# Kernel optimization log

Hardware: AMD Instinct MI355X
Metric: run time of the kernel (lower is better)

Reference implementation:

```python
import jax, jax.numpy as jnp
import numpy as np
from jax import lax

B = 64      # batch (n_image == n_caption)
R = 36      # image regions
W = 32      # words per caption (uniform cap_lens)
D = 1024    # embedding dim
LAMBDA_SOFTMAX = 9.0
LAMBDA_LSE = 6.0
ALPHA = 0.1
MARGIN = 0.2
OT_ITER = 20
BETA = 0.5
EPS = 1e-8


def setup_inputs() -> dict:
    key = jax.random.key(0)
    k1, k2, k3 = jax.random.split(key, 3)
    im = jax.random.normal(k1, (B, R, D), jnp.float32)
    s = jax.random.normal(k2, (B, W, D), jnp.float32)
    x = jax.random.normal(k3, (B, W, D), jnp.float32)
    s_l = jnp.full((B,), W, dtype=jnp.int32)
    return {"im": im, "s": s, "s_l": s_l, "x": x}


def _l2norm(a, axis):
    # matches torch l2norm: x / (sqrt(sum(x^2)) + eps)
    return a / (jnp.sqrt(jnp.sum(a * a, axis=axis, keepdims=True)) + EPS)


def _scores_t2i(im, s, x):
    # ---- func_attention (t2i): query = caption words, context = image regions ----
    # raw attn: (c, i, r, w) = context @ query^T for every caption/image pair
    attn = jnp.einsum('ird,cwd->cirw', im, s)
    attn = jax.nn.leaky_relu(attn, negative_slope=0.1)   # clipped_l2norm
    attn = _l2norm(attn, axis=3)                          # l2norm over query (word) axis
    attn = jnp.swapaxes(attn, 2, 3)                       # (c, i, w, r)
    attn = jax.nn.softmax(attn * LAMBDA_SOFTMAX, axis=3)  # softmax over regions
    wctx = jnp.einsum('ciwr,ird->ciwd', attn, im)         # weighted context (c,i,w,d)

    # cosine similarity between caption words and weighted context, over d
    num = jnp.einsum('cwd,ciwd->ciw', s, wctx)
    w1 = jnp.linalg.norm(s, axis=2)[:, None, :]           # (c,1,w)
    w2 = jnp.linalg.norm(wctx, axis=3)                    # (c,i,w)
    row_sim = num / jnp.maximum(w1 * w2, EPS)             # (c,i,w)

    # LogSumExp aggregation over words
    sim = jax.nn.logsumexp(row_sim * LAMBDA_LSE, axis=2) / LAMBDA_LSE  # (c,i)

    # ---- OT cost matrix: cosine distance between x words and image regions ----
    xn = x / (jnp.linalg.norm(x, axis=2, keepdims=True) + 1e-12)
    imn = im / (jnp.linalg.norm(im, axis=2, keepdims=True) + 1e-12)
    C = 1.0 - jnp.einsum('cwd,ird->ciwr', xn, imn)        # (c,i,W,R)

    # ---- IPOT (uniform marginals, beta=0.5, one inner step) ----
    A = jnp.exp(-C / BETA)
    T0 = jnp.ones_like(C)
    sigma0 = jnp.full(C.shape[:2] + (R,), 1.0 / R, dtype=C.dtype)

    def body(carry, _):
        T, sigma = carry
        Q = A * T                                          # (c,i,W,R)
        delta = 1.0 / (W * jnp.einsum('ciwr,cir->ciw', Q, sigma))
        sigma = 1.0 / (R * jnp.einsum('ciwr,ciw->cir', Q, delta))
        T = delta[..., :, None] * Q * sigma[..., None, :]
        return (T, sigma), None

    (T, _), _ = lax.scan(body, (T0, sigma0), None, length=OT_ITER)
    ot_dist = jnp.sum(C * T, axis=(-2, -1))               # trace(C^T T) -> (c,i)
    ot_sim = -ot_dist

    # torch code concatenates per-caption columns: scores[img, cap]
    return sim.T, ot_sim.T                                 # (n_img, n_cap)


def reference(im, s, s_l, x):
    # s_l is uniform (== W); the per-caption slicing in the torch loop is a no-op.
    scores, scores_ot = _scores_t2i(im, s, x)
    n = scores.shape[0]

    diag = jnp.diagonal(scores)
    diag_ot = jnp.diagonal(scores_ot)

    cost_s = jnp.maximum(MARGIN + scores - diag[:, None], 0.0)
    cost_im = jnp.maximum(MARGIN + scores - diag[None, :], 0.0)
    cost_s_ot = jnp.maximum(MARGIN + scores_ot - diag_ot[:, None], 0.0)
    cost_im_ot = jnp.maximum(MARGIN + scores_ot - diag_ot[None, :], 0.0)

    off = 1.0 - jnp.eye(n, dtype=scores.dtype)
    cost_s = cost_s * off
    cost_im = cost_im * off
    cost_s_ot = cost_s_ot * off
    cost_im_ot = cost_im_ot * off

    cost_s = cost_s + ALPHA * cost_s_ot
    cost_im = cost_im + ALPHA * cost_im_ot

    # max_violation = True
    cost_s = jnp.max(cost_s, axis=1)
    cost_im = jnp.max(cost_im, axis=0)
    cost_s_ot = jnp.max(cost_s_ot, axis=1)
    cost_im_ot = jnp.max(cost_im_ot, axis=0)

    return (jnp.sum(cost_s) + jnp.sum(cost_im),
            jnp.sum(cost_s_ot) + jnp.sum(cost_im_ot))
```

## Files before the change

kernel.cpp:

```cpp
#include <hip/hip_runtime.h>
#include <cstdint>
#include <cstddef>


typedef __attribute__((ext_vector_type(8))) short short8;
typedef __attribute__((ext_vector_type(4))) float f32x4;
typedef __attribute__((ext_vector_type(2))) float f2;

__device__ __forceinline__ unsigned short f2bf(float f) {
  unsigned u = __float_as_uint(f);
  u += 0x7FFFu + ((u >> 16) & 1u);
  return (unsigned short)(u >> 16);
}
__device__ __forceinline__ float rcpf(float x) { return __builtin_amdgcn_rcpf(x); }

__global__ __launch_bounds__(256) void k_prep(const float* __restrict__ s,
                                              const float* __restrict__ x,
                                              const float* __restrict__ im,
                                              unsigned short* __restrict__ Ab,
                                              unsigned short* __restrict__ Bb,
                                              float* __restrict__ w1,
                                              float* __restrict__ xn_r,
                                              float* __restrict__ imn_r) {
  int row = blockIdx.x, tid = threadIdx.x;
  const float* src; unsigned short* dst; float* np; int recip;
  if (row < 2048)      { src = s  + (size_t)row * 1024;          dst = Ab + (size_t)row * 1024;          np = w1    + row;          recip = 0; }
  else if (row < 4096) { src = x  + (size_t)(row - 2048) * 1024; dst = Ab + (size_t)row * 1024;          np = xn_r  + (row - 2048); recip = 1; }
  else                 { src = im + (size_t)(row - 4096) * 1024; dst = Bb + (size_t)(row - 4096) * 1024; np = imn_r + (row - 4096); recip = 1; }
  float4 f = ((const float4*)src)[tid];
  ushort4 h;
  h.x = f2bf(f.x); h.y = f2bf(f.y); h.z = f2bf(f.z); h.w = f2bf(f.w);
  ((ushort4*)dst)[tid] = h;
  float p = f.x*f.x + f.y*f.y + f.z*f.z + f.w*f.w;
  #pragma unroll
  for (int o = 32; o > 0; o >>= 1) p += __shfl_down(p, o, 64);
  __shared__ float red[4];
  if ((tid & 63) == 0) red[tid >> 6] = p;
  __syncthreads();
  if (tid == 0) {
    float n = sqrtf(red[0] + red[1] + red[2] + red[3]);
    *np = recip ? 1.f / (n + 1e-12f) : n;
  }
}

__global__ __launch_bounds__(256) void k_gram(const float* __restrict__ im,
                                              float* __restrict__ G) {
  int b = blockIdx.x, r = blockIdx.y;
  int wid = threadIdx.x >> 6, l = threadIdx.x & 63;
  const float* rowr = im + ((size_t)b*36 + r) * 1024;
  float4 my[4];
  #pragma unroll
  for (int j = 0; j < 4; ++j) my[j] = ((const float4*)rowr)[j*64 + l];
  float* Gr = G + ((size_t)b*36 + r) * 36;
  for (int rp = wid; rp < 36; rp += 4) {
    const float* rowp = im + ((size_t)b*36 + rp) * 1024;
    float p = 0.f;
    #pragma unroll
    for (int j = 0; j < 4; ++j) {
      float4 u = ((const float4*)rowp)[j*64 + l];
      p += my[j].x*u.x + my[j].y*u.y + my[j].z*u.z + my[j].w*u.w;
    }
    #pragma unroll
    for (int o = 32; o > 0; o >>= 1) p += __shfl_down(p, o, 64);
    if (l == 0) Gr[rp] = p;
  }
}

__global__ __launch_bounds__(256) void k_gemm_mfma(const unsigned short* __restrict__ A,
                                                   const unsigned short* __restrict__ B,
                                                   unsigned short* __restrict__ dot) {
  __shared__ unsigned short lA[128 * 32];
  __shared__ unsigned short lB[96 * 32];
  int tid = threadIdx.x;
  int bn = blockIdx.x * 96, bm = blockIdx.y * 128;
  int wid = tid >> 6, l = tid & 63;
  int wr = (wid >> 1) * 64, wc = (wid & 1) * 48;
  int lr = l & 15, lq = l >> 4;

  f32x4 acc[4][3] = {};

  int row_a = tid >> 2;
  int kq = (tid & 3) * 8;
  const unsigned short* gA = A + (size_t)(bm + row_a) * 1024 + kq;
  const unsigned short* gB = B + (size_t)(bn + row_a) * 1024 + kq;
  unsigned loff = (unsigned)tid * 16u;

  for (int kt = 0; kt < 1024; kt += 32) {
    __builtin_amdgcn_global_load_lds(
        (const __attribute__((address_space(1))) void*)(gA + kt),
        (__attribute__((address_space(3))) void*)((char*)lA + loff), 16, 0, 0);
    __builtin_amdgcn_global_load_lds(
        (const __attribute__((address_space(1))) void*)(gA + 64*1024 + kt),
        (__attribute__((address_space(3))) void*)((char*)lA + 4096 + loff), 16, 0, 0);
    __builtin_amdgcn_global_load_lds(
        (const __attribute__((address_space(1))) void*)(gB + kt),
        (__attribute__((address_space(3))) void*)((char*)lB + loff), 16, 0, 0);
    if (tid < 128)
      __builtin_amdgcn_global_load_lds(
          (const __attribute__((address_space(1))) void*)(gB + 64*1024 + kt),
          (__attribute__((address_space(3))) void*)((char*)lB + 4096 + loff), 16, 0, 0);
    __syncthreads();

    short8 af[4], bfr[3];
    #pragma unroll
    for (int mi = 0; mi < 4; ++mi)
      af[mi] = *(const short8*)&lA[(wr + mi*16 + lr) * 32 + lq * 8];
    #pragma unroll
    for (int ni = 0; ni < 3; ++ni)
      bfr[ni] = *(const short8*)&lB[(wc + ni*16 + lr) * 32 + lq * 8];
    #pragma unroll
    for (int mi = 0; mi < 4; ++mi)
      #pragma unroll
      for (int ni = 0; ni < 3; ++ni)
        acc[mi][ni] = __builtin_amdgcn_mfma_f32_16x16x32_bf16(af[mi], bfr[ni], acc[mi][ni], 0, 0, 0);
    __syncthreads();
  }

  #pragma unroll
  for (int mi = 0; mi < 4; ++mi)
    #pragma unroll
    for (int ni = 0; ni < 3; ++ni) {
      int gcol = bn + wc + ni*16 + lr;
      #pragma unroll
      for (int q = 0; q < 4; ++q) {
        int grow = bm + wr + mi*16 + lq*4 + q;
        dot[(size_t)grow * 2304 + gcol] = f2bf(acc[mi][ni][q]);
      }
    }
}

template<int C>
__device__ __forceinline__ float dpp_add(float v) {
  return v + __int_as_float(__builtin_amdgcn_mov_dpp(__float_as_int(v), C, 0xF, 0xF, true));
}
template<int C>
__device__ __forceinline__ float dpp_max(float v) {
  return fmaxf(v, __int_as_float(__builtin_amdgcn_mov_dpp(__float_as_int(v), C, 0xF, 0xF, true)));
}
__device__ __forceinline__ float bsum32(float v) {
  v = dpp_add<0xB1>(v);
  v = dpp_add<0x4E>(v);
  v = dpp_add<0x141>(v);
  v = dpp_add<0x128>(v);
  v += __shfl_xor(v, 16, 64);
  return v;
}
__device__ __forceinline__ float bmax32(float v) {
  v = dpp_max<0xB1>(v);
  v = dpp_max<0x4E>(v);
  v = dpp_max<0x141>(v);
  v = dpp_max<0x128>(v);
  v = fmaxf(v, __shfl_xor(v, 16, 64));
  return v;
}

__global__ __launch_bounds__(256, 4) void k_pair(const unsigned short* __restrict__ dotb,
                                                 const float* __restrict__ Gm,
                                                 const float* __restrict__ w1m,
                                                 const float* __restrict__ xnrm,
                                                 const float* __restrict__ imnrm,
                                                 float* __restrict__ S,
                                                 float* __restrict__ Sot) {
  int wid  = threadIdx.x >> 6;
  int pair = blockIdx.x * 4 + wid;
  int c = pair >> 6, i = pair & 63;
  int l = threadIdx.x & 63;
  int h = l >> 5, w = l & 31;
  int r0 = h * 18;

  const unsigned* drow = (const unsigned*)(dotb + (size_t)(c*32 + w) * 2304 + i*36 + r0);
  const unsigned* xrow = (const unsigned*)((const unsigned short*)drow + (size_t)2048 * 2304);
  float w1  = w1m[c*32 + w];
  float xnr = xnrm[c*32 + w];

  f2 d2[9], Cm2[9];
  #pragma unroll
  for (int k = 0; k < 9; ++k) {
    unsigned u = drow[k];
    d2[k][0] = __uint_as_float(u << 16);
    d2[k][1] = __uint_as_float(u & 0xFFFF0000u);
  }
  const f2* ir = (const f2*)(imnrm + i*36 + r0);
  #pragma unroll
  for (int k = 0; k < 9; ++k) {
    unsigned u = xrow[k];
    f2 xv;
    xv[0] = __uint_as_float(u << 16);
    xv[1] = __uint_as_float(u & 0xFFFF0000u);
    xv *= xnr;
    Cm2[k] = 1.f - xv * ir[k];
  }

  f2 f[9];
  #pragma unroll
  for (int k = 0; k < 9; ++k) {
    f2 t = d2[k] * 0.1f;
    f[k][0] = fmaxf(d2[k][0], t[0]);
    f[k][1] = fmaxf(d2[k][1], t[1]);
  }
  f2 p2[9];
  #pragma unroll
  for (int k = 0; k < 9; ++k) {
    f2 sq = f[k] * f[k];
    float t0 = bsum32(sq[0]);
    float t1 = bsum32(sq[1]);
    f2 rs;
    rs[0] = __builtin_amdgcn_rsqf(fmaxf(t0 * 0.012345679f, 1e-30f));
    rs[1] = __builtin_amdgcn_rsqf(fmaxf(t1 * 0.012345679f, 1e-30f));
    p2[k] = f[k] * rs;
  }
  float mx = fmaxf(fmaxf(p2[0][0], p2[0][1]), fmaxf(p2[1][0], p2[1][1]));
  #pragma unroll
  for (int k = 2; k < 9; ++k) mx = fmaxf(mx, fmaxf(p2[k][0], p2[k][1]));
  mx = fmaxf(mx, __shfl_xor(mx, 32, 64));

  f2 e2[9];
  f2 sum2 = {0.f, 0.f}, nu2 = {0.f, 0.f};
  #pragma unroll
  for (int k = 0; k < 9; ++k) {
    e2[k][0] = __expf(p2[k][0] - mx);
    e2[k][1] = __expf(p2[k][1] - mx);
    sum2 += e2[k];
    nu2 += e2[k] * d2[k];
  }
  float sum = sum2[0] + sum2[1];
  float numu = nu2[0] + nu2[1];
  sum  += __shfl_xor(sum, 32, 64);
  numu += __shfl_xor(numu, 32, 64);
  float inv = rcpf(sum);
  float num = numu * inv;

  f2 afull[18];
  #pragma unroll
  for (int k = 0; k < 9; ++k) {
    f2 a = e2[k] * inv;
    f2 o;
    o[0] = __shfl_xor(a[0], 32, 64);
    o[1] = __shfl_xor(a[1], 32, 64);
    afull[k][0]     = h ? o[0] : a[0];
    afull[k][1]     = h ? o[1] : a[1];
    afull[9 + k][0] = h ? a[0] : o[0];
    afull[9 + k][1] = h ? a[1] : o[1];
  }

  int iu = __builtin_amdgcn_readfirstlane(i);
  const float* Gi = Gm + (size_t)iu * 1296;
  float w2sq = 0.f;
  #pragma unroll 4
  for (int rp = 0; rp < 36; ++rp) {
    const f2* Gr = (const f2*)(Gi + rp * 36);
    f2 in2 = {0.f, 0.f};
    #pragma unroll
    for (int q = 0; q < 18; ++q) in2 += Gr[q] * afull[q];
    float ar = (rp & 1) ? afull[rp >> 1][1] : afull[rp >> 1][0];
    w2sq = fmaf(ar, in2[0] + in2[1], w2sq);
  }
  float w2 = __builtin_amdgcn_sqrtf(w2sq);
  float rs6 = 6.f * num * rcpf(fmaxf(w1 * w2, 1e-8f));

  float mw = bmax32(rs6);
  float se = bsum32(__expf(rs6 - mw));
  float sim = (mw + __logf(se)) * (1.f / 6.f);
  if (l == 0) S[i*64 + c] = sim;

  f2 Am2[9], Qm2[9], sg2[9];
  #pragma unroll
  for (int k = 0; k < 9; ++k) {
    Am2[k][0] = __expf(-2.f * Cm2[k][0]);
    Am2[k][1] = __expf(-2.f * Cm2[k][1]);
    Qm2[k] = Am2[k];
    sg2[k] = (f2){1.f/36.f, 1.f/36.f};
  }
  float delta = 0.f;
  for (int it = 0; it < 20; ++it) {
    f2 t2 = {0.f, 0.f};
    #pragma unroll
    for (int k = 0; k < 9; ++k) t2 += Qm2[k] * sg2[k];
    float tt = t2[0] + t2[1];
    tt += __shfl_xor(tt, 32, 64);
    delta = rcpf(32.f * tt);
    #pragma unroll
    for (int k = 0; k < 9; ++k) {
      f2 qd = Qm2[k] * delta;
      float q0 = bsum32(qd[0]);
      float q1 = bsum32(qd[1]);
      sg2[k][0] = rcpf(36.f * q0);
      sg2[k][1] = rcpf(36.f * q1);
    }
    if (it < 19) {
      #pragma unroll
      for (int k = 0; k < 9; ++k) Qm2[k] = (Am2[k] * delta) * Qm2[k] * sg2[k];
    }
  }
  f2 ot2 = {0.f, 0.f};
  #pragma unroll
  for (int k = 0; k < 9; ++k) ot2 += Cm2[k] * (Qm2[k] * delta * sg2[k]);
  float ot = ot2[0] + ot2[1];
  ot += __shfl_xor(ot, 32, 64);
  ot = bsum32(ot);
  if (l == 0) Sot[i*64 + c] = -ot;
}

__global__ __launch_bounds__(256) void k_reduce(const float* __restrict__ Sg,
                                                const float* __restrict__ Sotg,
                                                float* __restrict__ outp) {
  __shared__ float s[4096];
  __shared__ float so[4096];
  __shared__ float red0[256], red1[256];
  int tid = threadIdx.x;
  for (int e = tid; e < 4096; e += 256) { s[e] = Sg[e]; so[e] = Sotg[e]; }
  __syncthreads();
  float m0 = 0.f, m1 = 0.f;
  if (tid < 64) {
    int i = tid;
    float di = s[i*65], dio = so[i*65];
    for (int c2 = 0; c2 < 64; ++c2) {
      if (c2 == i) continue;
      float cs  = fmaxf(0.2f + s[i*64 + c2]  - di,  0.f);
      float cso = fmaxf(0.2f + so[i*64 + c2] - dio, 0.f);
      m0 = fmaxf(m0, cs + 0.1f * cso);
      m1 = fmaxf(m1, cso);
    }
  } else if (tid < 128) {
    int c2 = tid - 64;
    float dc = s[c2*65], dco = so[c2*65];
    for (int i = 0; i < 64; ++i) {
      if (i == c2) continue;
      float cim  = fmaxf(0.2f + s[i*64 + c2]  - dc,  0.f);
      float cimo = fmaxf(0.2f + so[i*64 + c2] - dco, 0.f);
      m0 = fmaxf(m0, cim + 0.1f * cimo);
      m1 = fmaxf(m1, cimo);
    }
  }
  red0[tid] = m0; red1[tid] = m1;
  __syncthreads();
  if (tid == 0) {
    float a0 = 0.f, a1 = 0.f;
    for (int t = 0; t < 128; ++t) { a0 += red0[t]; a1 += red1[t]; }
    outp[0] = a0;
    outp[1] = a1;
  }
}

extern "C" void kernel_launch(void* const* d_in, const int* in_sizes, int n_in,
                              void* d_out, int out_size, void* d_ws, size_t ws_size,
                              hipStream_t stream) {
  (void)in_sizes; (void)n_in; (void)out_size; (void)ws_size;
  const float* im = (const float*)d_in[0];
  const float* s  = (const float*)d_in[1];
  const float* x  = (const float*)d_in[3];
  float* out = (float*)d_out;

  unsigned short* Ab   = (unsigned short*)d_ws;
  unsigned short* Bb   = Ab + (size_t)4096 * 1024;
  unsigned short* dotb = Bb + (size_t)2304 * 1024;
  float* G     = (float*)(dotb + (size_t)4096 * 2304);
  float* w1    = G + 64*36*36;
  float* xn_r  = w1 + 2048;
  float* imn_r = xn_r + 2048;
  float* S     = imn_r + 2304;
  float* Sot   = S + 4096;

  k_prep<<<dim3(6400), 256, 0, stream>>>(s, x, im, Ab, Bb, w1, xn_r, imn_r);
  k_gemm_mfma<<<dim3(24, 32), 256, 0, stream>>>(Ab, Bb, dotb);
  k_gram<<<dim3(64, 36), 256, 0, stream>>>(im, G);
  k_pair<<<dim3(1024), 256, 0, stream>>>(dotb, G, w1, xn_r, imn_r, S, Sot);
  k_reduce<<<dim3(1), 256, 0, stream>>>(S, Sot, out);
}
```

Baseline: 116.6 us.

## Fold Gram computation into prep kernel and split pair kernel into score and IPOT

The Gram-matrix computation moves into the prep kernel as extra blocks, which removes one kernel launch and lets Gram work overlap with the bf16 conversion. The fused per-pair kernel is split into two kernels, one for the attention score and one for the IPOT transport score. Each of the new kernels holds fewer live registers, which may raise occupancy or cut spills. In exchange there is an extra launch and the per-pair indexing is duplicated across the two kernels.

```diff
diff --git a/kernel.cpp b/kernel.cpp
--- a/kernel.cpp
+++ b/kernel.cpp
@@ -21,8 +21,32 @@
                                               unsigned short* __restrict__ Bb,
                                               float* __restrict__ w1,
                                               float* __restrict__ xn_r,
-                                              float* __restrict__ imn_r) {
-  int row = blockIdx.x, tid = threadIdx.x;
+                                              float* __restrict__ imn_r,
+                                              float* __restrict__ G) {
+  int blk = blockIdx.x;
+  if (blk < 2304) {
+    int b = blk / 36, r = blk - b * 36;
+    int wid = threadIdx.x >> 6, l = threadIdx.x & 63;
+    const float* rowr = im + ((size_t)b*36 + r) * 1024;
+    float4 my[4];
+    #pragma unroll
+    for (int j = 0; j < 4; ++j) my[j] = ((const float4*)rowr)[j*64 + l];
+    float* Gr = G + ((size_t)b*36 + r) * 36;
+    for (int rp = wid; rp < 36; rp += 4) {
+      const float* rowp = im + ((size_t)b*36 + rp) * 1024;
+      float p = 0.f;
+      #pragma unroll
+      for (int j = 0; j < 4; ++j) {
+        float4 u = ((const float4*)rowp)[j*64 + l];
+        p += my[j].x*u.x + my[j].y*u.y + my[j].z*u.z + my[j].w*u.w;
+      }
+      #pragma unroll
+      for (int o = 32; o > 0; o >>= 1) p += __shfl_down(p, o, 64);
+      if (l == 0) Gr[rp] = p;
+    }
+    return;
+  }
+  int row = blk - 2304, tid = threadIdx.x;
   const float* src; unsigned short* dst; float* np; int recip;
   if (row < 2048)      { src = s  + (size_t)row * 1024;          dst = Ab + (size_t)row * 1024;          np = w1    + row;          recip = 0; }
   else if (row < 4096) { src = x  + (size_t)(row - 2048) * 1024; dst = Ab + (size_t)row * 1024;          np = xn_r  + (row - 2048); recip = 1; }
@@ -40,29 +64,6 @@
   if (tid == 0) {
     float n = sqrtf(red[0] + red[1] + red[2] + red[3]);
     *np = recip ? 1.f / (n + 1e-12f) : n;
-  }
-}
-
-__global__ __launch_bounds__(256) void k_gram(const float* __restrict__ im,
-                                              float* __restrict__ G) {
-  int b = blockIdx.x, r = blockIdx.y;
-  int wid = threadIdx.x >> 6, l = threadIdx.x & 63;
-  const float* rowr = im + ((size_t)b*36 + r) * 1024;
-  float4 my[4];
-  #pragma unroll
-  for (int j = 0; j < 4; ++j) my[j] = ((const float4*)rowr)[j*64 + l];
-  float* Gr = G + ((size_t)b*36 + r) * 36;
-  for (int rp = wid; rp < 36; rp += 4) {
-    const float* rowp = im + ((size_t)b*36 + rp) * 1024;
-    float p = 0.f;
-    #pragma unroll
-    for (int j = 0; j < 4; ++j) {
-      float4 u = ((const float4*)rowp)[j*64 + l];
-      p += my[j].x*u.x + my[j].y*u.y + my[j].z*u.z + my[j].w*u.w;
-    }
-    #pragma unroll
-    for (int o = 32; o > 0; o >>= 1) p += __shfl_down(p, o, 64);
-    if (l == 0) Gr[rp] = p;
   }
 }
 
@@ -154,13 +155,10 @@
   return v;
 }
 
-__global__ __launch_bounds__(256, 4) void k_pair(const unsigned short* __restrict__ dotb,
-                                                 const float* __restrict__ Gm,
-                                                 const float* __restrict__ w1m,
-                                                 const float* __restrict__ xnrm,
-                                                 const float* __restrict__ imnrm,
-                                                 float* __restrict__ S,
-                                                 float* __restrict__ Sot) {
+__global__ __launch_bounds__(256, 4) void k_score(const unsigned short* __restrict__ dotb,
+                                                  const float* __restrict__ Gm,
+                                                  const float* __restrict__ w1m,
+                                                  float* __restrict__ S) {
   int wid  = threadIdx.x >> 6;
   int pair = blockIdx.x * 4 + wid;
   int c = pair >> 6, i = pair & 63;
@@ -169,45 +167,30 @@
   int r0 = h * 18;
 
   const unsigned* drow = (const unsigned*)(dotb + (size_t)(c*32 + w) * 2304 + i*36 + r0);
-  const unsigned* xrow = (const unsigned*)((const unsigned short*)drow + (size_t)2048 * 2304);
-  float w1  = w1m[c*32 + w];
-  float xnr = xnrm[c*32 + w];
-
-  f2 d2[9], Cm2[9];
+  float w1 = w1m[c*32 + w];
+
+  f2 d2[9];
   #pragma unroll
   for (int k = 0; k < 9; ++k) {
     unsigned u = drow[k];
     d2[k][0] = __uint_as_float(u << 16);
     d2[k][1] = __uint_as_float(u & 0xFFFF0000u);
   }
-  const f2* ir = (const f2*)(imnrm + i*36 + r0);
-  #pragma unroll
-  for (int k = 0; k < 9; ++k) {
-    unsigned u = xrow[k];
-    f2 xv;
-    xv[0] = __uint_as_float(u << 16);
-    xv[1] = __uint_as_float(u & 0xFFFF0000u);
-    xv *= xnr;
-    Cm2[k] = 1.f - xv * ir[k];
-  }
-
-  f2 f[9];
+
+  f2 p2[9];
   #pragma unroll
   for (int k = 0; k < 9; ++k) {
     f2 t = d2[k] * 0.1f;
-    f[k][0] = fmaxf(d2[k][0], t[0]);
-    f[k][1] = fmaxf(d2[k][1], t[1]);
-  }
-  f2 p2[9];
-  #pragma unroll
-  for (int k = 0; k < 9; ++k) {
-    f2 sq = f[k] * f[k];
+    f2 fv;
+    fv[0] = fmaxf(d2[k][0], t[0]);
+    fv[1] = fmaxf(d2[k][1], t[1]);
+    f2 sq = fv * fv;
     float t0 = bsum32(sq[0]);
     float t1 = bsum32(sq[1]);
     f2 rs;
     rs[0] = __builtin_amdgcn_rsqf(fmaxf(t0 * 0.012345679f, 1e-30f));
     rs[1] = __builtin_amdgcn_rsqf(fmaxf(t1 * 0.012345679f, 1e-30f));
-    p2[k] = f[k] * rs;
+    p2[k] = fv * rs;
   }
   float mx = fmaxf(fmaxf(p2[0][0], p2[0][1]), fmaxf(p2[1][0], p2[1][1]));
   #pragma unroll
@@ -262,6 +245,33 @@
   float se = bsum32(__expf(rs6 - mw));
   float sim = (mw + __logf(se)) * (1.f / 6.f);
   if (l == 0) S[i*64 + c] = sim;
+}
+
+__global__ __launch_bounds__(256, 4) void k_ipot(const unsigned short* __restrict__ dotb,
+                                                 const float* __restrict__ xnrm,
+                                                 const float* __restrict__ imnrm,
+                                                 float* __restrict__ Sot) {
+  int wid  = threadIdx.x >> 6;
+  int pair = blockIdx.x * 4 + wid;
+  int c = pair >> 6, i = pair & 63;
+  int l = threadIdx.x & 63;
+  int h = l >> 5, w = l & 31;
+  int r0 = h * 18;
+
+  const unsigned* xrow = (const unsigned*)(dotb + (size_t)(2048 + c*32 + w) * 2304 + i*36 + r0);
+  float xnr = xnrm[c*32 + w];
+
+  f2 Cm2[9];
+  const f2* ir = (const f2*)(imnrm + i*36 + r0);
+  #pragma unroll
+  for (int k = 0; k < 9; ++k) {
+    unsigned u = xrow[k];
+    f2 xv;
+    xv[0] = __uint_as_float(u << 16);
+    xv[1] = __uint_as_float(u & 0xFFFF0000u);
+    xv *= xnr;
+    Cm2[k] = 1.f - xv * ir[k];
+  }
 
   f2 Am2[9], Qm2[9], sg2[9];
   #pragma unroll
@@ -361,9 +371,9 @@
   float* S     = imn_r + 2304;
   float* Sot   = S + 4096;
 
-  k_prep<<<dim3(6400), 256, 0, stream>>>(s, x, im, Ab, Bb, w1, xn_r, imn_r);
+  k_prep<<<dim3(8704), 256, 0, stream>>>(s, x, im, Ab, Bb, w1, xn_r, imn_r, G);
   k_gemm_mfma<<<dim3(24, 32), 256, 0, stream>>>(Ab, Bb, dotb);
-  k_gram<<<dim3(64, 36), 256, 0, stream>>>(im, G);
-  k_pair<<<dim3(1024), 256, 0, stream>>>(dotb, G, w1, xn_r, imn_r, S, Sot);
+  k_ipot<<<dim3(1024), 256, 0, stream>>>(dotb, xn_r, imn_r, Sot);
+  k_score<<<dim3(1024), 256, 0, stream>>>(dotb, G, w1, S);
   k_reduce<<<dim3(1), 256, 0, stream>>>(S, Sot, out);
 }
```

Measured after the change: 122.8 us. 5.3% more time.
